# Optimization experiments

Measured on AMD Instinct MI355X. Metric: run time of the kernel, lower is better.

Reference implementation:

```python
import jax, jax.numpy as jnp
import numpy as np

B, C, H, W = 8, 512, 64, 64
CQ = C // 8


def conv1x1(x, w, b):
    # x: [B,C,H,W], w: [O,C], b: [O] -> [B,O,H,W]
    return jnp.einsum('bchw,oc->bohw', x, w) + b[None, :, None, None]


def setup_inputs() -> dict:
    key = jax.random.key(0)
    ks = jax.random.split(key, 9)
    sc = 0.05
    return {
        'x2': jax.random.normal(ks[0], (B, C, H, W), jnp.float32),
        'x1': jax.random.normal(ks[1], (B, C, H, W), jnp.float32),
        'q_w': jax.random.normal(ks[2], (CQ, C), jnp.float32) * sc,
        'q_b': jax.random.normal(ks[3], (CQ,), jnp.float32) * sc,
        'k_w': jax.random.normal(ks[4], (CQ, C), jnp.float32) * sc,
        'k_b': jax.random.normal(ks[5], (CQ,), jnp.float32) * sc,
        'v_w': jax.random.normal(ks[6], (C, C), jnp.float32) * sc,
        'v_b': jax.random.normal(ks[7], (C,), jnp.float32) * sc,
        'gamma': jax.random.normal(ks[8], (1,), jnp.float32) * sc,
    }


def reference(x2, x1, q_w, q_b, k_w, k_b, v_w, v_b, gamma):
    h = x2.shape[2]
    q = conv1x1(x2, q_w, q_b)   # [B,CQ,H,W]
    k = conv1x1(x2, k_w, k_b)   # [B,CQ,H,W]
    v2 = conv1x1(x2, v_w, v_b)  # [B,C,H,W]
    v1 = conv1x1(x1, v_w, v_b)  # [B,C,H,W]

    # column (H) attention scores: query at (h,w) vs keys in same column
    energy_H = jnp.einsum('bchw,bcHw->bhwH', q, k)   # [B,H,W,H]
    # row (W) attention scores: query at (h,w) vs keys in same row
    energy_W = jnp.einsum('bchw,bchW->bhwW', q, k)   # [B,H,W,W]
    # NOTE: this module variant does NOT add the diagonal -inf mask.
    concate = jax.nn.softmax(jnp.concatenate([energy_H, energy_W], axis=3), axis=3)
    att_H = concate[..., :h]    # [B,H,W,H]
    att_W = concate[..., h:]    # [B,H,W,W]

    out_H2 = jnp.einsum('bcHw,bhwH->bchw', v2, att_H)
    out_W2 = jnp.einsum('bchW,bhwW->bchw', v2, att_W)
    out_H1 = jnp.einsum('bcHw,bhwH->bchw', v1, att_H)
    out_W1 = jnp.einsum('bchW,bhwW->bchw', v1, att_W)

    g = gamma[0]
    y2 = g * (out_H2 + out_W2) + x2
    y1 = g * (out_H1 + out_W1) + x1
    return (y2, y1)
```

## Files before the change

kernel.cpp:

```cpp
#include <hip/hip_runtime.h>
#include <cstdint>
#include <cstddef>

using u16 = unsigned short;
using u32 = unsigned int;

#define DI __device__ __forceinline__

typedef __attribute__((ext_vector_type(8))) short bf16x8;
typedef __attribute__((ext_vector_type(4))) float f32x4;

DI float bfu2f(u16 u) { return __uint_as_float(((u32)u) << 16); }
DI u16 f2bu(float f) {
    u32 x = __float_as_uint(f);
    return (u16)((x + 0x7fffu + ((x >> 16) & 1u)) >> 16);
}
DI u32 pk2(float a, float b) { return (u32)f2bu(a) | ((u32)f2bu(b) << 16); }

constexpr int CIN = 512;
constexpr int HW  = 4096;
constexpr size_t PLANE = 16777216ull;

__global__ __launch_bounds__(256) void proj_mfma(
    const float* __restrict__ X,
    const float* __restrict__ w0, const float* __restrict__ b0, int n0r,
    const float* __restrict__ w1, const float* __restrict__ b1, int n1r,
    const float* __restrict__ w2, const float* __restrict__ b2,
    u16* __restrict__ o0, u16* __restrict__ o1, u16* __restrict__ o2,
    int o0c, int o1c, int o2c)
{
    __shared__ u16 Wlds[128][40];
    __shared__ u16 Xlds[32][136];
    const int tid = threadIdx.x;
    const int m0  = blockIdx.y * 128;
    const int n0g = blockIdx.x * 128;
    const int b    = n0g >> 12;
    const int col0 = n0g & 4095;
    const float* Xb = X + (size_t)b * CIN * HW;

    const int ml = tid >> 1, wk0 = (tid & 1) * 16;
    const int xk = tid >> 3, xnb = (tid & 7) * 16;
    const int mrow = m0 + ml;
    const float* wr = (mrow < n0r) ? w0 + (size_t)mrow * CIN
                    : (mrow < n0r + n1r) ? w1 + (size_t)(mrow - n0r) * CIN
                    : w2 + (size_t)(mrow - n0r - n1r) * CIN;

    const int lane = tid & 63, wv = tid >> 6;
    const int wm = (wv & 1) * 64, wn = (wv >> 1) * 64;
    const int lr = lane & 15, lq = lane >> 4;

    f32x4 acc[4][4] = {};
    for (int kt = 0; kt < CIN; kt += 32) {
        {
            const float* p = wr + kt + wk0;
            float4 f0 = *(const float4*)(p);
            float4 f1 = *(const float4*)(p + 4);
            float4 f2 = *(const float4*)(p + 8);
            float4 f3 = *(const float4*)(p + 12);
            uint4 u0 = { pk2(f0.x, f0.y), pk2(f0.z, f0.w), pk2(f1.x, f1.y), pk2(f1.z, f1.w) };
            uint4 u1 = { pk2(f2.x, f2.y), pk2(f2.z, f2.w), pk2(f3.x, f3.y), pk2(f3.z, f3.w) };
            *(uint4*)&Wlds[ml][wk0]     = u0;
            *(uint4*)&Wlds[ml][wk0 + 8] = u1;
        }
        {
            const float* p = Xb + (size_t)(kt + xk) * HW + col0 + xnb;
            float4 f0 = *(const float4*)(p);
            float4 f1 = *(const float4*)(p + 4);
            float4 f2 = *(const float4*)(p + 8);
            float4 f3 = *(const float4*)(p + 12);
            uint4 u0 = { pk2(f0.x, f0.y), pk2(f0.z, f0.w), pk2(f1.x, f1.y), pk2(f1.z, f1.w) };
            uint4 u1 = { pk2(f2.x, f2.y), pk2(f2.z, f2.w), pk2(f3.x, f3.y), pk2(f3.z, f3.w) };
            *(uint4*)&Xlds[xk][xnb]     = u0;
            *(uint4*)&Xlds[xk][xnb + 8] = u1;
        }
        __syncthreads();
        bf16x8 a[4];
        #pragma unroll
        for (int i = 0; i < 4; i++)
            a[i] = *(const bf16x8*)&Wlds[wm + i * 16 + lr][lq * 8];
        #pragma unroll
        for (int j = 0; j < 4; j++) {
            bf16x8 bv;
            const int nn = wn + j * 16 + lr;
            #pragma unroll
            for (int jj = 0; jj < 8; jj++) bv[jj] = (short)Xlds[lq * 8 + jj][nn];
            #pragma unroll
            for (int i = 0; i < 4; i++)
                acc[i][j] = __builtin_amdgcn_mfma_f32_16x16x32_bf16(a[i], bv, acc[i][j], 0, 0, 0);
        }
        __syncthreads();
    }
    #pragma unroll
    for (int i = 0; i < 4; i++) {
        const int mbase = m0 + wm + i * 16;
        const float* bp; u16* op; int ch0, cc;
        if (mbase < n0r)             { bp = b0; op = o0; ch0 = mbase;             cc = o0c; }
        else if (mbase < n0r + n1r)  { bp = b1; op = o1; ch0 = mbase - n0r;       cc = o1c; }
        else                         { bp = b2; op = o2; ch0 = mbase - n0r - n1r; cc = o2c; }
        #pragma unroll
        for (int r = 0; r < 4; r++) {
            const int ch = ch0 + lq * 4 + r;
            const float bias = bp[ch];
            #pragma unroll
            for (int j = 0; j < 4; j++) {
                const int colx = col0 + wn + j * 16 + lr;
                op[((size_t)b * cc + ch) * HW + colx] = f2bu(acc[i][j][r] + bias);
            }
        }
    }
}

__global__ __launch_bounds__(256) void transpose64_bb(
    const u16* __restrict__ src, u16* __restrict__ dst)
{
    __shared__ u16 t[64][65];
    const size_t s = blockIdx.x;
    const u16* sp = src + s * 4096;
    u16* dp = dst + s * 4096;
    const int tid = threadIdx.x;
    #pragma unroll
    for (int i = 0; i < 16; i++) { int idx = tid + 256 * i; t[idx >> 6][idx & 63] = sp[idx]; }
    __syncthreads();
    #pragma unroll
    for (int i = 0; i < 16; i++) { int idx = tid + 256 * i; dp[idx] = t[idx & 63][idx >> 6]; }
}

__global__ __launch_bounds__(256) void transpose64_bb_inplace(u16* __restrict__ d)
{
    __shared__ u16 t[64][65];
    u16* p = d + (size_t)blockIdx.x * 4096;
    const int tid = threadIdx.x;
    #pragma unroll
    for (int i = 0; i < 16; i++) { int idx = tid + 256 * i; t[idx >> 6][idx & 63] = p[idx]; }
    __syncthreads();
    #pragma unroll
    for (int i = 0; i < 16; i++) { int idx = tid + 256 * i; p[idx] = t[idx & 63][idx >> 6]; }
}

__global__ __launch_bounds__(256) void transpose_cl(
    const u16* __restrict__ src, u16* __restrict__ dst)
{
    __shared__ u16 t[64][65];
    const int s = blockIdx.x;
    const int batch = s >> 6, tile = s & 63;
    const u16* sp = src + (size_t)batch * 262144 + (size_t)tile * 64;
    u16* dp = dst + (size_t)batch * 262144 + (size_t)tile * 4096;
    const int tid = threadIdx.x;
    {
        const int c = tid >> 2, x0 = (tid & 3) * 16;
        *(uint4*)&t[c][x0]     = *(const uint4*)(sp + (size_t)c * 4096 + x0);
        *(uint4*)&t[c][x0 + 8] = *(const uint4*)(sp + (size_t)c * 4096 + x0 + 8);
    }
    __syncthreads();
    {
        const int x = tid >> 2, c0 = (tid & 3) * 16;
        u16 tmp[16];
        #pragma unroll
        for (int i = 0; i < 16; i++) tmp[i] = t[c0 + i][x];
        *(uint4*)&dp[(size_t)x * 64 + c0]     = *(uint4*)&tmp[0];
        *(uint4*)&dp[(size_t)x * 64 + c0 + 8] = *(uint4*)&tmp[8];
    }
}

__global__ __launch_bounds__(256) void energy_h_mfma(
    const u16* __restrict__ qc, const u16* __restrict__ kc, float* __restrict__ e)
{
    __shared__ u16 Qs[64][72], Ks[64][72];
    const int w = blockIdx.x, b = blockIdx.y;
    const int tid = threadIdx.x;
    {
        const int row = tid >> 2, ch = (tid & 3) * 16;
        const size_t g = ((size_t)b * 4096 + (size_t)row * 64 + w) * 64 + ch;
        *(uint4*)&Qs[row][ch]     = *(const uint4*)(qc + g);
        *(uint4*)&Qs[row][ch + 8] = *(const uint4*)(qc + g + 8);
        *(uint4*)&Ks[row][ch]     = *(const uint4*)(kc + g);
        *(uint4*)&Ks[row][ch + 8] = *(const uint4*)(kc + g + 8);
    }
    __syncthreads();
    const int lane = tid & 63, wv = tid >> 6;
    const int mH = (wv & 1) * 32, nh = (wv >> 1) * 32;
    const int lr = lane & 15, lq = lane >> 4;
    f32x4 acc[2][2] = {};
    #pragma unroll
    for (int kt = 0; kt < 2; kt++) {
        const int k0 = kt * 32 + lq * 8;
        bf16x8 afr[2], bfr[2];
        #pragma unroll
        for (int i = 0; i < 2; i++) afr[i] = *(const bf16x8*)&Ks[mH + i * 16 + lr][k0];
        #pragma unroll
        for (int j = 0; j < 2; j++) bfr[j] = *(const bf16x8*)&Qs[nh + j * 16 + lr][k0];
        #pragma unroll
        for (int j = 0; j < 2; j++)
            #pragma unroll
            for (int i = 0; i < 2; i++)
                acc[i][j] = __builtin_amdgcn_mfma_f32_16x16x32_bf16(afr[i], bfr[j], acc[i][j], 0, 0, 0);
    }
    #pragma unroll
    for (int i = 0; i < 2; i++)
        #pragma unroll
        for (int j = 0; j < 2; j++) {
            const int h = nh + j * 16 + lr;
            const int Hp = mH + i * 16 + lq * 4;
            float4 v = make_float4(acc[i][j][0], acc[i][j][1], acc[i][j][2], acc[i][j][3]);
            *reinterpret_cast<float4*>(e + ((size_t)(b * 64 + h) * 64 + w) * 128 + Hp) = v;
        }
}

__global__ __launch_bounds__(256) void energy_w_mfma(
    const u16* __restrict__ qc, const u16* __restrict__ kc, float* __restrict__ e)
{
    __shared__ u16 Qs[64][72], Ks[64][72];
    const int h = blockIdx.x, b = blockIdx.y;
    const int tid = threadIdx.x;
    {
        const int row = tid >> 2, ch = (tid & 3) * 16;
        const size_t g = ((size_t)b * 4096 + (size_t)h * 64 + row) * 64 + ch;
        *(uint4*)&Qs[row][ch]     = *(const uint4*)(qc + g);
        *(uint4*)&Qs[row][ch + 8] = *(const uint4*)(qc + g + 8);
        *(uint4*)&Ks[row][ch]     = *(const uint4*)(kc + g);
        *(uint4*)&Ks[row][ch + 8] = *(const uint4*)(kc + g + 8);
    }
    __syncthreads();
    const int lane = tid & 63, wv = tid >> 6;
    const int mW = (wv & 1) * 32, nw = (wv >> 1) * 32;
    const int lr = lane & 15, lq = lane >> 4;
    f32x4 acc[2][2] = {};
    #pragma unroll
    for (int kt = 0; kt < 2; kt++) {
        const int k0 = kt * 32 + lq * 8;
        bf16x8 afr[2], bfr[2];
        #pragma unroll
        for (int i = 0; i < 2; i++) afr[i] = *(const bf16x8*)&Ks[mW + i * 16 + lr][k0];
        #pragma unroll
        for (int j = 0; j < 2; j++) bfr[j] = *(const bf16x8*)&Qs[nw + j * 16 + lr][k0];
        #pragma unroll
        for (int j = 0; j < 2; j++)
            #pragma unroll
            for (int i = 0; i < 2; i++)
                acc[i][j] = __builtin_amdgcn_mfma_f32_16x16x32_bf16(afr[i], bfr[j], acc[i][j], 0, 0, 0);
    }
    #pragma unroll
    for (int i = 0; i < 2; i++)
        #pragma unroll
        for (int j = 0; j < 2; j++) {
            const int w = nw + j * 16 + lr;
            const int Wp = mW + i * 16 + lq * 4;
            float4 v = make_float4(acc[i][j][0], acc[i][j][1], acc[i][j][2], acc[i][j][3]);
            *reinterpret_cast<float4*>(e + ((size_t)(b * 64 + h) * 64 + w) * 128 + 64 + Wp) = v;
        }
}

__global__ __launch_bounds__(256) void softmax128_bf(
    const float* __restrict__ e, u16* __restrict__ attb)
{
    const int pos = blockIdx.x * 4 + (threadIdx.x >> 6);
    const int l = threadIdx.x & 63;
    const float* p = e + (size_t)pos * 128;
    float v0 = p[l], v1 = p[l + 64];
    float m = fmaxf(v0, v1);
    #pragma unroll
    for (int o = 32; o > 0; o >>= 1) m = fmaxf(m, __shfl_xor(m, o, 64));
    float e0 = __expf(v0 - m), e1 = __expf(v1 - m);
    float s = e0 + e1;
    #pragma unroll
    for (int o = 32; o > 0; o >>= 1) s += __shfl_xor(s, o, 64);
    float inv = 1.0f / s;
    u16* q = attb + (size_t)pos * 128;
    q[l] = f2bu(e0 * inv);
    q[l + 64] = f2bu(e1 * inv);
}

__global__ __launch_bounds__(256) void agg_h_mfma(
    const u16* __restrict__ vTa, const u16* __restrict__ vTb,
    const u16* __restrict__ attb, u16* __restrict__ Pa, u16* __restrict__ Pb)
{
    __shared__ u16 Vs[128][72];
    __shared__ u16 As[64][72];
    const int mt = blockIdx.x, w = blockIdx.y, b = blockIdx.z;
    const u16* vT = (mt < 4) ? vTa : vTb;
    u16*       P  = (mt < 4) ? Pa  : Pb;
    const int c0 = (mt & 3) * 128;
    const int tid = threadIdx.x;
    const u16* va = vT + ((size_t)(b * 512 + c0) * 64 + w) * 64;
    const u16* ab = attb + ((size_t)b * 4096 + w) * 128;
    {
        const int r = tid >> 3, cB = (tid & 7) * 8;
        #pragma unroll
        for (int i = 0; i < 4; i++)
            *(uint4*)&Vs[r + 32 * i][cB] = *(const uint4*)(va + (size_t)(r + 32 * i) * 4096 + cB);
        #pragma unroll
        for (int i = 0; i < 2; i++)
            *(uint4*)&As[r + 32 * i][cB] = *(const uint4*)(ab + (size_t)(r + 32 * i) * 8192 + cB);
    }
    __syncthreads();
    const int lane = tid & 63, wv = tid >> 6;
    const int wh = (wv & 1) * 32, wc = (wv >> 1) * 64;
    const int lr = lane & 15, lq = lane >> 4;
    f32x4 acc[2][4] = {};
    #pragma unroll
    for (int kt = 0; kt < 2; kt++) {
        const int k0 = kt * 32 + lq * 8;
        bf16x8 afr[2], bfr[4];
        #pragma unroll
        for (int i = 0; i < 2; i++) afr[i] = *(const bf16x8*)&As[wh + i * 16 + lr][k0];
        #pragma unroll
        for (int j = 0; j < 4; j++) bfr[j] = *(const bf16x8*)&Vs[wc + j * 16 + lr][k0];
        #pragma unroll
        for (int j = 0; j < 4; j++)
            #pragma unroll
            for (int i = 0; i < 2; i++)
                acc[i][j] = __builtin_amdgcn_mfma_f32_16x16x32_bf16(afr[i], bfr[j], acc[i][j], 0, 0, 0);
    }
    #pragma unroll
    for (int i = 0; i < 2; i++)
        #pragma unroll
        for (int j = 0; j < 4; j++) {
            const int c = c0 + wc + j * 16 + lr;
            const int hb = wh + i * 16 + lq * 4;
            uint2 pkd = { pk2(acc[i][j][0], acc[i][j][1]), pk2(acc[i][j][2], acc[i][j][3]) };
            *(uint2*)(P + (size_t)(b * 512 + c) * 4096 + (size_t)w * 64 + hb) = pkd;
        }
}

__global__ __launch_bounds__(256) void agg_w_mfma(
    const u16* __restrict__ v2, const u16* __restrict__ v1,
    const u16* __restrict__ P2, const u16* __restrict__ P1,
    const u16* __restrict__ attb,
    const float* __restrict__ x2, const float* __restrict__ x1,
    const float* __restrict__ gptr, float* __restrict__ out)
{
    __shared__ u16 Vs[128][72];
    __shared__ u16 As[64][72];
    const int mt = blockIdx.x, h = blockIdx.y, b = blockIdx.z;
    const u16* v = (mt < 4) ? v2 : v1;
    const u16* P = (mt < 4) ? P2 : P1;
    const float* x = (mt < 4) ? x2 : x1;
    float* y = out + ((mt < 4) ? 0 : PLANE);
    const int c0 = (mt & 3) * 128;
    const int tid = threadIdx.x;
    const u16* vb = v + (size_t)(b * 512 + c0) * 4096 + h * 64;
    const u16* ab = attb + ((size_t)(b * 64 + h) * 64) * 128 + 64;
    {
        const int r = tid >> 3, cB = (tid & 7) * 8;
        #pragma unroll
        for (int i = 0; i < 4; i++)
            *(uint4*)&Vs[r + 32 * i][cB] = *(const uint4*)(vb + (size_t)(r + 32 * i) * 4096 + cB);
        #pragma unroll
        for (int i = 0; i < 2; i++)
            *(uint4*)&As[r + 32 * i][cB] = *(const uint4*)(ab + (size_t)(r + 32 * i) * 128 + cB);
    }
    __syncthreads();
    const int lane = tid & 63, wv = tid >> 6;
    const int ww = (wv & 1) * 32, wc = (wv >> 1) * 64;
    const int lr = lane & 15, lq = lane >> 4;
    f32x4 acc[2][4] = {};
    #pragma unroll
    for (int kt = 0; kt < 2; kt++) {
        const int k0 = kt * 32 + lq * 8;
        bf16x8 afr[2], bfr[4];
        #pragma unroll
        for (int i = 0; i < 2; i++) afr[i] = *(const bf16x8*)&As[ww + i * 16 + lr][k0];
        #pragma unroll
        for (int j = 0; j < 4; j++) bfr[j] = *(const bf16x8*)&Vs[wc + j * 16 + lr][k0];
        #pragma unroll
        for (int j = 0; j < 4; j++)
            #pragma unroll
            for (int i = 0; i < 2; i++)
                acc[i][j] = __builtin_amdgcn_mfma_f32_16x16x32_bf16(afr[i], bfr[j], acc[i][j], 0, 0, 0);
    }
    const float g = gptr[0];
    #pragma unroll
    for (int i = 0; i < 2; i++)
        #pragma unroll
        for (int j = 0; j < 4; j++) {
            const int c = c0 + wc + j * 16 + lr;
            const int wb = ww + i * 16 + lq * 4;
            const size_t o = (size_t)(b * 512 + c) * 4096 + (size_t)h * 64 + wb;
            float4 xv = *reinterpret_cast<const float4*>(x + o);
            u32 p01 = ((const u32*)(P + o))[0];
            u32 p23 = ((const u32*)(P + o))[1];
            float4 yv;
            yv.x = g * (bfu2f((u16)(p01 & 0xffff)) + acc[i][j][0]) + xv.x;
            yv.y = g * (bfu2f((u16)(p01 >> 16))    + acc[i][j][1]) + xv.y;
            yv.z = g * (bfu2f((u16)(p23 & 0xffff)) + acc[i][j][2]) + xv.z;
            yv.w = g * (bfu2f((u16)(p23 >> 16))    + acc[i][j][3]) + xv.w;
            *reinterpret_cast<float4*>(y + o) = yv;
        }
}

extern "C" void kernel_launch(void* const* d_in, const int* in_sizes, int n_in,
                              void* d_out, int out_size, void* d_ws, size_t ws_size,
                              hipStream_t stream)
{
    (void)in_sizes; (void)n_in; (void)out_size; (void)ws_size;
    const float* x2  = (const float*)d_in[0];
    const float* x1  = (const float*)d_in[1];
    const float* q_w = (const float*)d_in[2];
    const float* q_b = (const float*)d_in[3];
    const float* k_w = (const float*)d_in[4];
    const float* k_b = (const float*)d_in[5];
    const float* v_w = (const float*)d_in[6];
    const float* v_b = (const float*)d_in[7];
    const float* gm  = (const float*)d_in[8];

    char* ws = (char*)d_ws;
    u16*   v2   = (u16*)(ws);
    u16*   v1   = (u16*)(ws + ((size_t)32  << 20));
    u16*   attb = (u16*)(ws + ((size_t)64  << 20));
    u16*   q    = (u16*)(ws + ((size_t)72  << 20));
    u16*   k    = (u16*)(ws + ((size_t)76  << 20));
    u16*   qc   = (u16*)(ws + ((size_t)80  << 20));
    u16*   kc   = (u16*)(ws + ((size_t)84  << 20));
    float* e    = (float*)(ws + ((size_t)88 << 20));
    u16*   vT2  = (u16*)(ws + ((size_t)72  << 20));
    u16*   vT1  = (u16*)(ws + ((size_t)104 << 20));
    float* out = (float*)d_out;

    dim3 blk(256);
    proj_mfma<<<dim3(256, 5), blk, 0, stream>>>(x2, q_w, q_b, 64, k_w, k_b, 64,
                                                v_w, v_b, q, k, v2, 64, 64, 512);
    proj_mfma<<<dim3(256, 4), blk, 0, stream>>>(x1, v_w, v_b, 0, v_w, v_b, 0,
                                                v_w, v_b, q, k, v1, 64, 64, 512);
    transpose_cl<<<1024, blk, 0, stream>>>(q, qc);
    energy_h_mfma<<<dim3(64, 8), blk, 0, stream>>>(qc, kc, e);
    energy_w_mfma<<<dim3(64, 8), blk, 0, stream>>>(qc, kc, e);
    softmax128_bf<<<8192, blk, 0, stream>>>(e, attb);
    transpose64_bb<<<8192, blk, 0, stream>>>(v2, vT2);
    agg_h_mfma<<<dim3(8, 64, 8), blk, 0, stream>>>(vT2, vT1, attb, vT2, vT1);
    transpose64_bb_inplace<<<8192, blk, 0, stream>>>(vT2);
    agg_w_mfma<<<dim3(8, 64, 8), blk, 0, stream>>>(v2, v1, vT2, vT1, attb,
                                                   x2, x1, gm, out);
}
```

Baseline: 519.3 us.

## Halve channel tile in aggregation kernels and swap MFMA operands for coalesced stores

In both aggregation kernels the channel tile per block drops from 128 to 64, which doubles the grid. The MFMA operand roles are swapped so that V supplies the A operand and attention the B operand. As a result, each lane's accumulator rows now run along channels, and the 16 lanes of a group write contiguous spatial positions. The epilogues change from per-lane 16-byte vector stores scattered across channels to scalar stores that are contiguous across lanes, aiming at better global-memory coalescing and more parallelism. The trade-off is more redundant loads of attention tiles and narrower per-thread stores.

After: 530.6 us. +2.2%, slower.

```diff
diff --git a/kernel.cpp b/kernel.cpp
--- a/kernel.cpp
+++ b/kernel.cpp
@@ -274,19 +274,19 @@
     const u16* __restrict__ vTa, const u16* __restrict__ vTb,
     const u16* __restrict__ attb, u16* __restrict__ Pa, u16* __restrict__ Pb)
 {
-    __shared__ u16 Vs[128][72];
+    __shared__ u16 Vs[64][72];
     __shared__ u16 As[64][72];
     const int mt = blockIdx.x, w = blockIdx.y, b = blockIdx.z;
-    const u16* vT = (mt < 4) ? vTa : vTb;
-    u16*       P  = (mt < 4) ? Pa  : Pb;
-    const int c0 = (mt & 3) * 128;
+    const u16* vT = (mt < 8) ? vTa : vTb;
+    u16*       P  = (mt < 8) ? Pa  : Pb;
+    const int c0 = (mt & 7) * 64;
     const int tid = threadIdx.x;
     const u16* va = vT + ((size_t)(b * 512 + c0) * 64 + w) * 64;
     const u16* ab = attb + ((size_t)b * 4096 + w) * 128;
     {
         const int r = tid >> 3, cB = (tid & 7) * 8;
         #pragma unroll
-        for (int i = 0; i < 4; i++)
+        for (int i = 0; i < 2; i++)
             *(uint4*)&Vs[r + 32 * i][cB] = *(const uint4*)(va + (size_t)(r + 32 * i) * 4096 + cB);
         #pragma unroll
         for (int i = 0; i < 2; i++)
@@ -294,19 +294,19 @@
     }
     __syncthreads();
     const int lane = tid & 63, wv = tid >> 6;
-    const int wh = (wv & 1) * 32, wc = (wv >> 1) * 64;
+    const int wc = (wv & 1) * 32, wh = (wv >> 1) * 32;
     const int lr = lane & 15, lq = lane >> 4;
-    f32x4 acc[2][4] = {};
+    f32x4 acc[2][2] = {};
     #pragma unroll
     for (int kt = 0; kt < 2; kt++) {
         const int k0 = kt * 32 + lq * 8;
-        bf16x8 afr[2], bfr[4];
-        #pragma unroll
-        for (int i = 0; i < 2; i++) afr[i] = *(const bf16x8*)&As[wh + i * 16 + lr][k0];
-        #pragma unroll
-        for (int j = 0; j < 4; j++) bfr[j] = *(const bf16x8*)&Vs[wc + j * 16 + lr][k0];
-        #pragma unroll
-        for (int j = 0; j < 4; j++)
+        bf16x8 afr[2], bfr[2];
+        #pragma unroll
+        for (int i = 0; i < 2; i++) afr[i] = *(const bf16x8*)&Vs[wc + i * 16 + lr][k0];
+        #pragma unroll
+        for (int j = 0; j < 2; j++) bfr[j] = *(const bf16x8*)&As[wh + j * 16 + lr][k0];
+        #pragma unroll
+        for (int j = 0; j < 2; j++)
             #pragma unroll
             for (int i = 0; i < 2; i++)
                 acc[i][j] = __builtin_amdgcn_mfma_f32_16x16x32_bf16(afr[i], bfr[j], acc[i][j], 0, 0, 0);
@@ -314,11 +314,10 @@
     #pragma unroll
     for (int i = 0; i < 2; i++)
         #pragma unroll
-        for (int j = 0; j < 4; j++) {
-            const int c = c0 + wc + j * 16 + lr;
-            const int hb = wh + i * 16 + lq * 4;
-            uint2 pkd = { pk2(acc[i][j][0], acc[i][j][1]), pk2(acc[i][j][2], acc[i][j][3]) };
-            *(uint2*)(P + (size_t)(b * 512 + c) * 4096 + (size_t)w * 64 + hb) = pkd;
+        for (int j = 0; j < 2; j++) {
+            u16* pp = P + ((size_t)(b * 512 + c0 + wc + i * 16 + lq * 4) * 64 + w) * 64 + wh + j * 16 + lr;
+            #pragma unroll
+            for (int r = 0; r < 4; r++) pp[(size_t)r * 4096] = f2bu(acc[i][j][r]);
         }
 }
 
@@ -329,21 +328,21 @@
     const float* __restrict__ x2, const float* __restrict__ x1,
     const float* __restrict__ gptr, float* __restrict__ out)
 {
-    __shared__ u16 Vs[128][72];
+    __shared__ u16 Vs[64][72];
     __shared__ u16 As[64][72];
     const int mt = blockIdx.x, h = blockIdx.y, b = blockIdx.z;
-    const u16* v = (mt < 4) ? v2 : v1;
-    const u16* P = (mt < 4) ? P2 : P1;
-    const float* x = (mt < 4) ? x2 : x1;
-    float* y = out + ((mt < 4) ? 0 : PLANE);
-    const int c0 = (mt & 3) * 128;
+    const u16* v = (mt < 8) ? v2 : v1;
+    const u16* P = (mt < 8) ? P2 : P1;
+    const float* x = (mt < 8) ? x2 : x1;
+    float* y = out + ((mt < 8) ? 0 : PLANE);
+    const int c0 = (mt & 7) * 64;
     const int tid = threadIdx.x;
     const u16* vb = v + (size_t)(b * 512 + c0) * 4096 + h * 64;
     const u16* ab = attb + ((size_t)(b * 64 + h) * 64) * 128 + 64;
     {
         const int r = tid >> 3, cB = (tid & 7) * 8;
         #pragma unroll
-        for (int i = 0; i < 4; i++)
+        for (int i = 0; i < 2; i++)
             *(uint4*)&Vs[r + 32 * i][cB] = *(const uint4*)(vb + (size_t)(r + 32 * i) * 4096 + cB);
         #pragma unroll
         for (int i = 0; i < 2; i++)
@@ -351,19 +350,19 @@
     }
     __syncthreads();
     const int lane = tid & 63, wv = tid >> 6;
-    const int ww = (wv & 1) * 32, wc = (wv >> 1) * 64;
+    const int wc = (wv & 1) * 32, ww = (wv >> 1) * 32;
     const int lr = lane & 15, lq = lane >> 4;
-    f32x4 acc[2][4] = {};
+    f32x4 acc[2][2] = {};
     #pragma unroll
     for (int kt = 0; kt < 2; kt++) {
         const int k0 = kt * 32 + lq * 8;
-        bf16x8 afr[2], bfr[4];
-        #pragma unroll
-        for (int i = 0; i < 2; i++) afr[i] = *(const bf16x8*)&As[ww + i * 16 + lr][k0];
-        #pragma unroll
-        for (int j = 0; j < 4; j++) bfr[j] = *(const bf16x8*)&Vs[wc + j * 16 + lr][k0];
-        #pragma unroll
-        for (int j = 0; j < 4; j++)
+        bf16x8 afr[2], bfr[2];
+        #pragma unroll
+        for (int i = 0; i < 2; i++) afr[i] = *(const bf16x8*)&Vs[wc + i * 16 + lr][k0];
+        #pragma unroll
+        for (int j = 0; j < 2; j++) bfr[j] = *(const bf16x8*)&As[ww + j * 16 + lr][k0];
+        #pragma unroll
+        for (int j = 0; j < 2; j++)
             #pragma unroll
             for (int i = 0; i < 2; i++)
                 acc[i][j] = __builtin_amdgcn_mfma_f32_16x16x32_bf16(afr[i], bfr[j], acc[i][j], 0, 0, 0);
@@ -372,19 +371,14 @@
     #pragma unroll
     for (int i = 0; i < 2; i++)
         #pragma unroll
-        for (int j = 0; j < 4; j++) {
-            const int c = c0 + wc + j * 16 + lr;
-            const int wb = ww + i * 16 + lq * 4;
-            const size_t o = (size_t)(b * 512 + c) * 4096 + (size_t)h * 64 + wb;
-            float4 xv = *reinterpret_cast<const float4*>(x + o);
-            u32 p01 = ((const u32*)(P + o))[0];
-            u32 p23 = ((const u32*)(P + o))[1];
-            float4 yv;
-            yv.x = g * (bfu2f((u16)(p01 & 0xffff)) + acc[i][j][0]) + xv.x;
-            yv.y = g * (bfu2f((u16)(p01 >> 16))    + acc[i][j][1]) + xv.y;
-            yv.z = g * (bfu2f((u16)(p23 & 0xffff)) + acc[i][j][2]) + xv.z;
-            yv.w = g * (bfu2f((u16)(p23 >> 16))    + acc[i][j][3]) + xv.w;
-            *reinterpret_cast<float4*>(y + o) = yv;
+        for (int j = 0; j < 2; j++) {
+            size_t off = (size_t)(b * 512 + c0 + wc + i * 16 + lq * 4) * 4096
+                       + (size_t)h * 64 + ww + j * 16 + lr;
+            #pragma unroll
+            for (int r = 0; r < 4; r++) {
+                size_t o = off + (size_t)r * 4096;
+                y[o] = g * (bfu2f(P[o]) + acc[i][j][r]) + x[o];
+            }
         }
 }
 
@@ -426,8 +420,8 @@
     energy_w_mfma<<<dim3(64, 8), blk, 0, stream>>>(qc, kc, e);
     softmax128_bf<<<8192, blk, 0, stream>>>(e, attb);
     transpose64_bb<<<8192, blk, 0, stream>>>(v2, vT2);
-    agg_h_mfma<<<dim3(8, 64, 8), blk, 0, stream>>>(vT2, vT1, attb, vT2, vT1);
+    agg_h_mfma<<<dim3(16, 64, 8), blk, 0, stream>>>(vT2, vT1, attb, vT2, vT1);
     transpose64_bb_inplace<<<8192, blk, 0, stream>>>(vT2);
-    agg_w_mfma<<<dim3(8, 64, 8), blk, 0, stream>>>(v2, v1, vT2, vT1, attb,
-                                                   x2, x1, gm, out);
-}
+    agg_w_mfma<<<dim3(16, 64, 8), blk, 0, stream>>>(v2, v1, vT2, vT1, attb,
+                                                    x2, x1, gm, out);
+}
```

## Merge projection launches and transpose MFMA operand roles for coalesced stores

Applied to the files above, without the earlier changes.

Folds the two projection launches into one 9-row grid that picks x2 or x1 per block. X is now staged K-contiguous in LDS, so B fragments become single vector LDS reads instead of eight scalar gathers. The MFMA operand roles are swapped so outputs come out as packed uint2 along the spatial axis. The aggregation kernels also swap operand roles, which turns their epilogues into strided scalar stores and loads. The aim is to cut LDS gather cost and a launch, at the price of X global loads that are now column-strided per thread, possibly less coalesced.

Result: faster. 499.3 us (-3.8%).

```diff
diff --git a/kernel.cpp b/kernel.cpp
--- a/kernel.cpp
+++ b/kernel.cpp
@@ -22,90 +22,96 @@
 constexpr size_t PLANE = 16777216ull;
 
 __global__ __launch_bounds__(256) void proj_mfma(
-    const float* __restrict__ X,
-    const float* __restrict__ w0, const float* __restrict__ b0, int n0r,
-    const float* __restrict__ w1, const float* __restrict__ b1, int n1r,
-    const float* __restrict__ w2, const float* __restrict__ b2,
-    u16* __restrict__ o0, u16* __restrict__ o1, u16* __restrict__ o2,
-    int o0c, int o1c, int o2c)
+    const float* __restrict__ x2, const float* __restrict__ x1,
+    const float* __restrict__ q_w, const float* __restrict__ q_b,
+    const float* __restrict__ k_w, const float* __restrict__ k_b,
+    const float* __restrict__ v_w, const float* __restrict__ v_b,
+    u16* __restrict__ oq, u16* __restrict__ ok,
+    u16* __restrict__ ov2, u16* __restrict__ ov1)
 {
     __shared__ u16 Wlds[128][40];
-    __shared__ u16 Xlds[32][136];
+    __shared__ u16 Xlds[128][40];
     const int tid = threadIdx.x;
     const int m0  = blockIdx.y * 128;
     const int n0g = blockIdx.x * 128;
     const int b    = n0g >> 12;
     const int col0 = n0g & 4095;
-    const float* Xb = X + (size_t)b * CIN * HW;
-
-    const int ml = tid >> 1, wk0 = (tid & 1) * 16;
-    const int xk = tid >> 3, xnb = (tid & 7) * 16;
-    const int mrow = m0 + ml;
-    const float* wr = (mrow < n0r) ? w0 + (size_t)mrow * CIN
-                    : (mrow < n0r + n1r) ? w1 + (size_t)(mrow - n0r) * CIN
-                    : w2 + (size_t)(mrow - n0r - n1r) * CIN;
+    const float* Xb = ((m0 < 640) ? x2 : x1) + (size_t)b * CIN * HW;
+
+    const bool isX = tid < 128;
+    const int sr = tid & 127;
+    const int mrow = m0 + sr;
+    const float* wr;
+    if (mrow < 64)        wr = q_w + (size_t)mrow * CIN;
+    else if (mrow < 128)  wr = k_w + (size_t)(mrow - 64) * CIN;
+    else if (mrow < 640)  wr = v_w + (size_t)(mrow - 128) * CIN;
+    else                  wr = v_w + (size_t)(mrow - 640) * CIN;
 
     const int lane = tid & 63, wv = tid >> 6;
-    const int wm = (wv & 1) * 64, wn = (wv >> 1) * 64;
+    const int wn = (wv & 1) * 64;
+    const int wm = (wv >> 1) * 64;
     const int lr = lane & 15, lq = lane >> 4;
 
     f32x4 acc[4][4] = {};
     for (int kt = 0; kt < CIN; kt += 32) {
-        {
-            const float* p = wr + kt + wk0;
-            float4 f0 = *(const float4*)(p);
-            float4 f1 = *(const float4*)(p + 4);
-            float4 f2 = *(const float4*)(p + 8);
-            float4 f3 = *(const float4*)(p + 12);
-            uint4 u0 = { pk2(f0.x, f0.y), pk2(f0.z, f0.w), pk2(f1.x, f1.y), pk2(f1.z, f1.w) };
-            uint4 u1 = { pk2(f2.x, f2.y), pk2(f2.z, f2.w), pk2(f3.x, f3.y), pk2(f3.z, f3.w) };
-            *(uint4*)&Wlds[ml][wk0]     = u0;
-            *(uint4*)&Wlds[ml][wk0 + 8] = u1;
-        }
-        {
-            const float* p = Xb + (size_t)(kt + xk) * HW + col0 + xnb;
-            float4 f0 = *(const float4*)(p);
-            float4 f1 = *(const float4*)(p + 4);
-            float4 f2 = *(const float4*)(p + 8);
-            float4 f3 = *(const float4*)(p + 12);
-            uint4 u0 = { pk2(f0.x, f0.y), pk2(f0.z, f0.w), pk2(f1.x, f1.y), pk2(f1.z, f1.w) };
-            uint4 u1 = { pk2(f2.x, f2.y), pk2(f2.z, f2.w), pk2(f3.x, f3.y), pk2(f3.z, f3.w) };
-            *(uint4*)&Xlds[xk][xnb]     = u0;
-            *(uint4*)&Xlds[xk][xnb + 8] = u1;
+        if (isX) {
+            const float* px = Xb + (size_t)kt * HW + col0 + sr;
+            u32 pkv[16];
+            #pragma unroll
+            for (int kk = 0; kk < 16; kk++) {
+                float a = px[(size_t)(2 * kk) * HW];
+                float c = px[(size_t)(2 * kk + 1) * HW];
+                pkv[kk] = pk2(a, c);
+            }
+            *(uint4*)&Xlds[sr][0]  = *(uint4*)&pkv[0];
+            *(uint4*)&Xlds[sr][8]  = *(uint4*)&pkv[4];
+            *(uint4*)&Xlds[sr][16] = *(uint4*)&pkv[8];
+            *(uint4*)&Xlds[sr][24] = *(uint4*)&pkv[12];
+        } else {
+            const float* p = wr + kt;
+            u32 pw[16];
+            #pragma unroll
+            for (int t = 0; t < 8; t++) {
+                float4 f = *(const float4*)(p + 4 * t);
+                pw[2 * t]     = pk2(f.x, f.y);
+                pw[2 * t + 1] = pk2(f.z, f.w);
+            }
+            *(uint4*)&Wlds[sr][0]  = *(uint4*)&pw[0];
+            *(uint4*)&Wlds[sr][8]  = *(uint4*)&pw[4];
+            *(uint4*)&Wlds[sr][16] = *(uint4*)&pw[8];
+            *(uint4*)&Wlds[sr][24] = *(uint4*)&pw[12];
         }
         __syncthreads();
-        bf16x8 a[4];
+        bf16x8 a[4], bb[4];
         #pragma unroll
         for (int i = 0; i < 4; i++)
-            a[i] = *(const bf16x8*)&Wlds[wm + i * 16 + lr][lq * 8];
-        #pragma unroll
-        for (int j = 0; j < 4; j++) {
-            bf16x8 bv;
-            const int nn = wn + j * 16 + lr;
-            #pragma unroll
-            for (int jj = 0; jj < 8; jj++) bv[jj] = (short)Xlds[lq * 8 + jj][nn];
+            a[i] = *(const bf16x8*)&Xlds[wn + i * 16 + lr][lq * 8];
+        #pragma unroll
+        for (int j = 0; j < 4; j++)
+            bb[j] = *(const bf16x8*)&Wlds[wm + j * 16 + lr][lq * 8];
+        #pragma unroll
+        for (int j = 0; j < 4; j++)
             #pragma unroll
             for (int i = 0; i < 4; i++)
-                acc[i][j] = __builtin_amdgcn_mfma_f32_16x16x32_bf16(a[i], bv, acc[i][j], 0, 0, 0);
-        }
+                acc[i][j] = __builtin_amdgcn_mfma_f32_16x16x32_bf16(a[i], bb[j], acc[i][j], 0, 0, 0);
         __syncthreads();
     }
     #pragma unroll
-    for (int i = 0; i < 4; i++) {
-        const int mbase = m0 + wm + i * 16;
+    for (int j = 0; j < 4; j++) {
+        const int mbase = m0 + wm + j * 16;
         const float* bp; u16* op; int ch0, cc;
-        if (mbase < n0r)             { bp = b0; op = o0; ch0 = mbase;             cc = o0c; }
-        else if (mbase < n0r + n1r)  { bp = b1; op = o1; ch0 = mbase - n0r;       cc = o1c; }
-        else                         { bp = b2; op = o2; ch0 = mbase - n0r - n1r; cc = o2c; }
-        #pragma unroll
-        for (int r = 0; r < 4; r++) {
-            const int ch = ch0 + lq * 4 + r;
-            const float bias = bp[ch];
-            #pragma unroll
-            for (int j = 0; j < 4; j++) {
-                const int colx = col0 + wn + j * 16 + lr;
-                op[((size_t)b * cc + ch) * HW + colx] = f2bu(acc[i][j][r] + bias);
-            }
+        if (mbase < 64)       { bp = q_b; op = oq;  ch0 = mbase;       cc = 64;  }
+        else if (mbase < 128) { bp = k_b; op = ok;  ch0 = mbase - 64;  cc = 64;  }
+        else if (mbase < 640) { bp = v_b; op = ov2; ch0 = mbase - 128; cc = 512; }
+        else                  { bp = v_b; op = ov1; ch0 = mbase - 640; cc = 512; }
+        const int ch = ch0 + lr;
+        const float bias = bp[ch];
+        u16* obase = op + ((size_t)b * cc + ch) * HW + col0 + wn + lq * 4;
+        #pragma unroll
+        for (int i = 0; i < 4; i++) {
+            uint2 pkd = { pk2(acc[i][j][0] + bias, acc[i][j][1] + bias),
+                          pk2(acc[i][j][2] + bias, acc[i][j][3] + bias) };
+            *(uint2*)(obase + i * 16) = pkd;
         }
     }
 }
@@ -294,31 +300,30 @@
     }
     __syncthreads();
     const int lane = tid & 63, wv = tid >> 6;
-    const int wh = (wv & 1) * 32, wc = (wv >> 1) * 64;
+    const int wm = (wv & 1) * 64, wn = (wv >> 1) * 32;
     const int lr = lane & 15, lq = lane >> 4;
-    f32x4 acc[2][4] = {};
+    f32x4 acc[4][2] = {};
     #pragma unroll
     for (int kt = 0; kt < 2; kt++) {
         const int k0 = kt * 32 + lq * 8;
-        bf16x8 afr[2], bfr[4];
-        #pragma unroll
-        for (int i = 0; i < 2; i++) afr[i] = *(const bf16x8*)&As[wh + i * 16 + lr][k0];
-        #pragma unroll
-        for (int j = 0; j < 4; j++) bfr[j] = *(const bf16x8*)&Vs[wc + j * 16 + lr][k0];
-        #pragma unroll
-        for (int j = 0; j < 4; j++)
-            #pragma unroll
-            for (int i = 0; i < 2; i++)
+        bf16x8 afr[4], bfr[2];
+        #pragma unroll
+        for (int i = 0; i < 4; i++) afr[i] = *(const bf16x8*)&Vs[wm + i * 16 + lr][k0];
+        #pragma unroll
+        for (int j = 0; j < 2; j++) bfr[j] = *(const bf16x8*)&As[wn + j * 16 + lr][k0];
+        #pragma unroll
+        for (int j = 0; j < 2; j++)
+            #pragma unroll
+            for (int i = 0; i < 4; i++)
                 acc[i][j] = __builtin_amdgcn_mfma_f32_16x16x32_bf16(afr[i], bfr[j], acc[i][j], 0, 0, 0);
     }
     #pragma unroll
-    for (int i = 0; i < 2; i++)
-        #pragma unroll
-        for (int j = 0; j < 4; j++) {
-            const int c = c0 + wc + j * 16 + lr;
-            const int hb = wh + i * 16 + lq * 4;
-            uint2 pkd = { pk2(acc[i][j][0], acc[i][j][1]), pk2(acc[i][j][2], acc[i][j][3]) };
-            *(uint2*)(P + (size_t)(b * 512 + c) * 4096 + (size_t)w * 64 + hb) = pkd;
+    for (int i = 0; i < 4; i++)
+        #pragma unroll
+        for (int j = 0; j < 2; j++) {
+            u16* pp = P + ((size_t)(b * 512 + c0 + wm + i * 16 + lq * 4) * 64 + w) * 64 + wn + j * 16 + lr;
+            #pragma unroll
+            for (int r = 0; r < 4; r++) pp[(size_t)r * 4096] = f2bu(acc[i][j][r]);
         }
 }
 
@@ -351,40 +356,35 @@
     }
     __syncthreads();
     const int lane = tid & 63, wv = tid >> 6;
-    const int ww = (wv & 1) * 32, wc = (wv >> 1) * 64;
+    const int wm = (wv & 1) * 64, wn = (wv >> 1) * 32;
     const int lr = lane & 15, lq = lane >> 4;
-    f32x4 acc[2][4] = {};
+    f32x4 acc[4][2] = {};
     #pragma unroll
     for (int kt = 0; kt < 2; kt++) {
         const int k0 = kt * 32 + lq * 8;
-        bf16x8 afr[2], bfr[4];
-        #pragma unroll
-        for (int i = 0; i < 2; i++) afr[i] = *(const bf16x8*)&As[ww + i * 16 + lr][k0];
-        #pragma unroll
-        for (int j = 0; j < 4; j++) bfr[j] = *(const bf16x8*)&Vs[wc + j * 16 + lr][k0];
-        #pragma unroll
-        for (int j = 0; j < 4; j++)
-            #pragma unroll
-            for (int i = 0; i < 2; i++)
+        bf16x8 afr[4], bfr[2];
+        #pragma unroll
+        for (int i = 0; i < 4; i++) afr[i] = *(const bf16x8*)&Vs[wm + i * 16 + lr][k0];
+        #pragma unroll
+        for (int j = 0; j < 2; j++) bfr[j] = *(const bf16x8*)&As[wn + j * 16 + lr][k0];
+        #pragma unroll
+        for (int j = 0; j < 2; j++)
+            #pragma unroll
+            for (int i = 0; i < 4; i++)
                 acc[i][j] = __builtin_amdgcn_mfma_f32_16x16x32_bf16(afr[i], bfr[j], acc[i][j], 0, 0, 0);
     }
     const float g = gptr[0];
     #pragma unroll
-    for (int i = 0; i < 2; i++)
-        #pragma unroll
-        for (int j = 0; j < 4; j++) {
-            const int c = c0 + wc + j * 16 + lr;
-            const int wb = ww + i * 16 + lq * 4;
-            const size_t o = (size_t)(b * 512 + c) * 4096 + (size_t)h * 64 + wb;
-            float4 xv = *reinterpret_cast<const float4*>(x + o);
-            u32 p01 = ((const u32*)(P + o))[0];
-            u32 p23 = ((const u32*)(P + o))[1];
-            float4 yv;
-            yv.x = g * (bfu2f((u16)(p01 & 0xffff)) + acc[i][j][0]) + xv.x;
-            yv.y = g * (bfu2f((u16)(p01 >> 16))    + acc[i][j][1]) + xv.y;
-            yv.z = g * (bfu2f((u16)(p23 & 0xffff)) + acc[i][j][2]) + xv.z;
-            yv.w = g * (bfu2f((u16)(p23 >> 16))    + acc[i][j][3]) + xv.w;
-            *reinterpret_cast<float4*>(y + o) = yv;
+    for (int i = 0; i < 4; i++)
+        #pragma unroll
+        for (int j = 0; j < 2; j++) {
+            size_t off = (size_t)(b * 512 + c0 + wm + i * 16 + lq * 4) * 4096
+                       + (size_t)h * 64 + wn + j * 16 + lr;
+            #pragma unroll
+            for (int r = 0; r < 4; r++) {
+                size_t o = off + (size_t)r * 4096;
+                y[o] = g * (bfu2f(P[o]) + acc[i][j][r]) + x[o];
+            }
         }
 }
 
@@ -417,10 +417,8 @@
     float* out = (float*)d_out;
 
     dim3 blk(256);
-    proj_mfma<<<dim3(256, 5), blk, 0, stream>>>(x2, q_w, q_b, 64, k_w, k_b, 64,
-                                                v_w, v_b, q, k, v2, 64, 64, 512);
-    proj_mfma<<<dim3(256, 4), blk, 0, stream>>>(x1, v_w, v_b, 0, v_w, v_b, 0,
-                                                v_w, v_b, q, k, v1, 64, 64, 512);
+    proj_mfma<<<dim3(256, 9), blk, 0, stream>>>(x2, x1, q_w, q_b, k_w, k_b,
+                                                v_w, v_b, q, k, v2, v1);
     transpose_cl<<<1024, blk, 0, stream>>>(q, qc);
     energy_h_mfma<<<dim3(64, 8), blk, 0, stream>>>(qc, kc, e);
     energy_w_mfma<<<dim3(64, 8), blk, 0, stream>>>(qc, kc, e);
```
